# Kernel optimization log

Hardware: AMD Instinct MI355X
Metric: run time of the kernel (lower is better)

The kernel has to match this reference:

```python
import jax, jax.numpy as jnp
from jax import lax
import numpy as np

N_ATOMS, N_BONDS, N_GRAPHS = 8192, 32768, 256
EMBED, HIDDEN, DEPTH = 32, 256, 10
ATOM_VOCAB, BOND_VOCAB = 200, 10


def setup_inputs() -> dict:
    key = jax.random.key(0)
    ks = jax.random.split(key, 16)
    f = lambda k, *sh: jax.random.normal(k, sh, dtype=jnp.float32) * 0.05
    return {
        "atom_features": jax.random.randint(ks[0], (N_ATOMS,), 0, ATOM_VOCAB),
        "bond_features": jax.random.randint(ks[1], (N_BONDS,), 0, BOND_VOCAB),
        "adjacency_matrix": jax.random.randint(ks[2], (N_ATOMS, N_ATOMS), 0, 2, dtype=jnp.int32),
        "batch_indices": jax.random.randint(ks[3], (N_ATOMS,), 0, N_GRAPHS),
        "atom_emb": f(ks[4], ATOM_VOCAB, EMBED),
        "bond_emb": f(ks[5], BOND_VOCAB, EMBED),
        "msg_W": f(ks[6], DEPTH, HIDDEN, 2 * EMBED),
        "msg_b": f(ks[7], DEPTH, HIDDEN),
        "gru_Wih": f(ks[8], DEPTH, 3 * EMBED, HIDDEN),
        "gru_Whh": f(ks[9], DEPTH, 3 * EMBED, EMBED),
        "gru_bih": f(ks[10], DEPTH, 3 * EMBED),
        "gru_bhh": f(ks[11], DEPTH, 3 * EMBED),
        "pool_W": f(ks[12], HIDDEN, EMBED),
        "pool_b": f(ks[13], HIDDEN),
    }


def _gmpn(atom_emb, bond_emb, msg_W, msg_b, gru_Wih, gru_Whh, gru_bih, gru_bhh,
          pool_W, pool_b, atom_features, bond_features, adjacency_matrix, batch_indices):
    H = atom_emb[atom_features]                       # [N, E]
    A = (adjacency_matrix > 0).astype(H.dtype)        # [N, N] 0/1
    deg = A.sum(axis=1)                               # [N]
    has_nb = deg > 0
    inv_deg = jnp.where(has_nb, 1.0 / jnp.maximum(deg, 1.0), 0.0)[:, None]

    def layer(h, params):
        W, b, wih, whh, b_ih, b_hh = params
        # mean_j Linear([h_i ; h_j]) = W1 h_i + W2 mean_j h_j + b
        neigh_mean = (A @ h) * inv_deg                # [N, E]
        W1, W2 = W[:, :EMBED], W[:, EMBED:]
        msg = h @ W1.T + neigh_mean @ W2.T + b        # [N, HIDDEN]
        msg = jnp.where(has_nb[:, None], msg, 0.0)    # zero message if no neighbors
        # single-step GRU: input=msg, hidden state=h
        gi = msg @ wih.T + b_ih
        gh = h @ whh.T + b_hh
        ir, iz, inn = jnp.split(gi, 3, axis=-1)
        hr, hz, hn = jnp.split(gh, 3, axis=-1)
        r = jax.nn.sigmoid(ir + hr)
        z = jax.nn.sigmoid(iz + hz)
        n = jnp.tanh(inn + r * hn)
        h_new = (1.0 - z) * n + z * h                 # [N, E]
        return h_new, None

    H, _ = lax.scan(layer, H, (msg_W, msg_b, gru_Wih, gru_Whh, gru_bih, gru_bhh))

    # per-graph mean pooling (zeros for empty graphs), then global_pool linear
    seg_sum = jax.ops.segment_sum(H, batch_indices, num_segments=N_GRAPHS)
    cnt = jax.ops.segment_sum(jnp.ones((H.shape[0],), H.dtype), batch_indices, num_segments=N_GRAPHS)
    graph_mean = jnp.where(cnt[:, None] > 0, seg_sum / jnp.maximum(cnt, 1.0)[:, None], 0.0)
    graph_embeddings = graph_mean @ pool_W.T + pool_b  # [G, HIDDEN]

    bond_embeddings = bond_emb[bond_features]          # [B, E]
    return H, bond_embeddings, graph_embeddings


def reference(atom_features, bond_features, adjacency_matrix, batch_indices,
              atom_emb, bond_emb, msg_W, msg_b, gru_Wih, gru_Whh, gru_bih, gru_bhh,
              pool_W, pool_b):
    return _gmpn(atom_emb, bond_emb, msg_W, msg_b, gru_Wih, gru_Whh, gru_bih, gru_bhh,
                 pool_W, pool_b, atom_features, bond_features, adjacency_matrix, batch_indices)
```

## Files before the change

### kernel.cpp

```cpp
#include <hip/hip_runtime.h>
#include <stdint.h>

typedef __bf16 bf16x8 __attribute__((ext_vector_type(8)));
typedef float f32x4 __attribute__((ext_vector_type(4)));

__device__ __forceinline__ float b2f(unsigned short u){
  unsigned int t = ((unsigned int)u) << 16;
  return __builtin_bit_cast(float, t);
}
__device__ __forceinline__ unsigned short f2b(float f){
  unsigned int x = __builtin_bit_cast(unsigned int, f);
  x = x + 0x7FFFu + ((x >> 16) & 1u);
  return (unsigned short)(x >> 16);
}
__device__ __forceinline__ void spread8(unsigned int B, unsigned int w[4]){
  unsigned int m = __umul24(B, 0x8001u);
  w[0] = __umul24(m & 0x00010001u, 0x3F80u);
  w[1] = __umul24(m & 0x00040004u, 0x0FE0u);
  w[2] = __umul24(m & 0x00100010u, 0x03F8u);
  w[3] = __umul24(m & 0x00400040u, 0x00FEu);
}
__device__ __forceinline__ float fsig(float x){ return 1.f/(1.f + __expf(-x)); }
__device__ __forceinline__ float ftanh(float x){ return 1.f - 2.f/(__expf(2.f*x) + 1.f); }

__global__ void k_prep(const void* s_msgW, const void* s_msgb, const void* s_wih,
                       const void* s_whh, const void* s_bih, const void* s_bhh,
                       const void* s_poolW, const void* s_poolb,
                       const unsigned short* __restrict__ aemb_u16,
                       unsigned short* __restrict__ cw,
                       int* __restrict__ deg, float* __restrict__ seg,
                       float* __restrict__ cnt, int* __restrict__ flag){
  int b = blockIdx.x, t = threadIdx.x;
  unsigned int uu = aemb_u16[2*t];
  int e = (int)((uu >> 7) & 0xFF);
  unsigned long long vote = __ballot(e >= 100 && e <= 127);
  int isb = (__popcll(vote) > 32) ? 1 : 0;
  if (b < 1771){
    int id = b*256 + t;
    if (id < 453248){
      const void* src; int off;
      if      (id < 163840){ src = s_msgW;  off = id; }
      else if (id < 166400){ src = s_msgb;  off = id - 163840; }
      else if (id < 412160){ src = s_wih;   off = id - 166400; }
      else if (id < 442880){ src = s_whh;   off = id - 412160; }
      else if (id < 443840){ src = s_bih;   off = id - 442880; }
      else if (id < 444800){ src = s_bhh;   off = id - 443840; }
      else if (id < 452992){ src = s_poolW; off = id - 444800; }
      else                 { src = s_poolb; off = id - 452992; }
      cw[id] = isb ? ((const unsigned short*)src)[off]
                   : f2b(((const float*)src)[off]);
    }
  } else {
    int id2 = (b - 1771)*256 + t;
    if (id2 < 8192){ deg[id2] = 0; seg[id2] = 0.f; }
    if (id2 < 256) cnt[id2] = 0.f;
    if (b == 1771 && t == 0) flag[0] = isb;
  }
}

__global__ void k_fuse(const unsigned short* __restrict__ cw,
                       unsigned short* __restrict__ vcat, float* __restrict__ bwv){
  int d = blockIdx.x >> 2, quarter = blockIdx.x & 3;
  const unsigned short* msgW = cw + (size_t)d*16384;
  const unsigned short* msgb = cw + 163840 + d*256;
  const unsigned short* wih  = cw + 166400 + (size_t)d*24576;
  int t = threadIdx.x;
  #pragma unroll
  for (int i=0;i<6;i++){
    int idx = quarter*1536 + i*256 + t;
    int j = idx >> 6, e = idx & 63;
    const unsigned short* wr = wih + j*256;
    const unsigned short* wc = msgW + e;
    float acc = 0.f;
    for (int k=0;k<256;k++)
      acc += b2f(wr[k]) * b2f(wc[k*64]);
    vcat[(size_t)d*6144 + idx] = f2b(acc);
  }
  if (quarter == 0 && t < 96){
    const unsigned short* wr = wih + t*256;
    float acc = 0.f;
    for (int k=0;k<256;k++) acc += b2f(msgb[k]) * b2f(wr[k]);
    bwv[d*96 + t] = acc;
  }
}

__global__ void k_pack(const int* __restrict__ adj, unsigned int* __restrict__ mask3,
                       int* __restrict__ deg){
  int tid = blockIdx.x*256 + threadIdx.x;
  int rb  = tid >> 12;
  int rem = tid & 4095;
  int kgg = rem >> 6;
  int L   = rem & 63;
  int lc = L & 15, q = L >> 4;
  int row = rb*16 + lc;
  const int4* p4 = (const int4*)(adj + (size_t)row*8192 + kgg*128 + q*8);
  unsigned int dw = 0; int pc = 0;
  #pragma unroll
  for (int s=0;s<4;s++){
    int4 u = p4[s*8];
    int4 v = p4[s*8 + 1];
    unsigned int b = (unsigned int)(u.x > 0)
                   | ((unsigned int)(u.y > 0) << 1)
                   | ((unsigned int)(u.z > 0) << 2)
                   | ((unsigned int)(u.w > 0) << 3)
                   | ((unsigned int)(v.x > 0) << 4)
                   | ((unsigned int)(v.y > 0) << 5)
                   | ((unsigned int)(v.z > 0) << 6)
                   | ((unsigned int)(v.w > 0) << 7);
    dw |= b << (8*s);
    pc += __popc(b);
  }
  mask3[tid] = dw;
  pc += __shfl_xor(pc, 16);
  pc += __shfl_xor(pc, 32);
  if (q == 0) atomicAdd(deg + row, pc);
}

__global__ void k_be(const int* __restrict__ af, const void* __restrict__ araw,
                     const int* __restrict__ bft, const void* __restrict__ braw,
                     const int* __restrict__ flag,
                     float* __restrict__ hf32, uint4* __restrict__ hfrag,
                     unsigned short* __restrict__ outB16, float* __restrict__ outB32){
  int b = blockIdx.x, t = threadIdx.x;
  if (b >= 512){
    int id = (b - 512)*512 + t;
    int e = id >> 5, c = id & 31;
    int idx = bft[e]*32 + c;
    if (flag[0]) outB16[id] = ((const unsigned short*)braw)[idx];
    else         outB32[id] = ((const float*)braw)[idx];
    return;
  }
  __shared__ __align__(16) float sh[512];
  int r = t >> 5, c = t & 31;
  int row = b*16 + r;
  int idx = af[row]*32 + c;
  float f;
  if (flag[0]) f = b2f(((const unsigned short*)araw)[idx]);
  else         f = ((const float*)araw)[idx];
  hf32[row*32 + c] = f;
  sh[r*32 + c] = f;
  __syncthreads();
  if (t < 64){
    int nt = t >> 5, Lq = t & 31;
    int ks32 = b >> 1, half = b & 1;
    int col = nt*16 + (Lq & 15);
    int rbase = (Lq >> 4)*8;
    unsigned int w[4];
    #pragma unroll
    for (int p=0;p<4;p++){
      unsigned int lo = f2b(sh[(rbase + 2*p    )*32 + col]);
      unsigned int hi = f2b(sh[(rbase + 2*p + 1)*32 + col]);
      w[p] = lo | (hi << 16);
    }
    hfrag[(ks32*2 + nt)*64 + half*32 + Lq] = make_uint4(w[0],w[1],w[2],w[3]);
  }
}

__launch_bounds__(512, 1)
__global__ void k_layer(const unsigned int* __restrict__ mask3,
                        const uint4* __restrict__ hfragIn,
                        unsigned int* __restrict__ hfragOut,
                        float* __restrict__ hf32,
                        const int* __restrict__ deg,
                        const unsigned short* __restrict__ vcat,
                        const float* __restrict__ bwv,
                        const unsigned short* __restrict__ whh,
                        const unsigned short* __restrict__ bih,
                        const unsigned short* __restrict__ bhh,
                        const int* __restrict__ bidx,
                        float* __restrict__ seg, float* __restrict__ cnt,
                        unsigned short* __restrict__ out16, float* __restrict__ out32,
                        const int* __restrict__ flag, int last)
{
  __shared__ __align__(16) char uni[33792];
  __shared__ __align__(16) unsigned short sA[32][72];
  __shared__ int sdeg[32];

  const int t = threadIdx.x;
  const int b = blockIdx.x;
  const int w = t >> 6, L = t & 63;
  const int q = L >> 4, lc = L & 15;
  const int rowbase = b*32;

  const int r0 = t >> 4;
  const int cl = t & 15;
  const int r  = rowbase + r0;
  const int isb = flag[0];
  const int dgr = deg[r];
  const float invr = dgr > 0 ? 1.f/(float)dgr : 0.f;
  float h0 = hf32[r*32 + cl];
  float h1 = hf32[r*32 + 16 + cl];
  sA[r0][cl]    = f2b(h0);
  sA[r0][16+cl] = f2b(h1);
  if (cl == 0) sdeg[r0] = dgr;

  {
    f32x4 a00={0,0,0,0}, a01={0,0,0,0}, a10={0,0,0,0}, a11={0,0,0,0};
    const unsigned int* mp = mask3 + (size_t)b*8192 + w*512 + L;
    const uint4* bp = hfragIn + (size_t)w*4096 + L;
    for (int g=0; g<8; g++){
      unsigned int mw0 = mp[g*64];
      unsigned int mw1 = mp[4096 + g*64];
      #pragma unroll
      for (int s=0; s<4; s++){
        int ks = g*4 + s;
        uint4 u0 = bp[ks*128];
        uint4 u1 = bp[ks*128 + 64];
        union { unsigned int u[4]; bf16x8 v; } A0, A1, B0, B1;
        spread8((mw0 >> (8*s)) & 0xFFu, A0.u);
        spread8((mw1 >> (8*s)) & 0xFFu, A1.u);
        B0.u[0]=u0.x; B0.u[1]=u0.y; B0.u[2]=u0.z; B0.u[3]=u0.w;
        B1.u[0]=u1.x; B1.u[1]=u1.y; B1.u[2]=u1.z; B1.u[3]=u1.w;
        a00 = __builtin_amdgcn_mfma_f32_16x16x32_bf16(A0.v, B0.v, a00, 0,0,0);
        a01 = __builtin_amdgcn_mfma_f32_16x16x32_bf16(A0.v, B1.v, a01, 0,0,0);
        a10 = __builtin_amdgcn_mfma_f32_16x16x32_bf16(A1.v, B0.v, a10, 0,0,0);
        a11 = __builtin_amdgcn_mfma_f32_16x16x32_bf16(A1.v, B1.v, a11, 0,0,0);
      }
    }
    float* sp = (float*)uni + w*1056;
    #pragma unroll
    for (int rg=0; rg<4; rg++){
      int rw = q*4 + rg;
      sp[rw*33 + lc]         = a00[rg];
      sp[rw*33 + 16 + lc]    = a01[rg];
      sp[(16+rw)*33 + lc]    = a10[rg];
      sp[(16+rw)*33 + 16+lc] = a11[rg];
    }
  }
  __syncthreads();
  {
    const float* spf = (const float*)uni;
    float s0 = 0.f, s1 = 0.f;
    #pragma unroll
    for (int ww=0; ww<8; ww++){
      s0 += spf[ww*1056 + r0*33 + cl];
      s1 += spf[ww*1056 + r0*33 + 16 + cl];
    }
    sA[r0][32+cl] = f2b(s0*invr);
    sA[r0][48+cl] = f2b(s1*invr);
  }
  __syncthreads();
  {
    float* sgi = (float*)uni;
    float* sgh = (float*)(uni + 12800);
    if (w < 6){
      int nt = w;
      union { uint4 u; bf16x8 v; } B0, B1;
      B0.u = *(const uint4*)(vcat + (size_t)(nt*16 + lc)*64 + q*8);
      B1.u = *(const uint4*)(vcat + (size_t)(nt*16 + lc)*64 + 32 + q*8);
      float bw = bwv[nt*16 + lc];
      #pragma unroll
      for (int rt=0; rt<2; rt++){
        union { uint4 u; bf16x8 v; } A0, A1;
        A0.u = *(const uint4*)&sA[rt*16 + lc][q*8];
        A1.u = *(const uint4*)&sA[rt*16 + lc][32 + q*8];
        f32x4 g0 = {0,0,0,0};
        g0 = __builtin_amdgcn_mfma_f32_16x16x32_bf16(A0.v, B0.v, g0, 0,0,0);
        g0 = __builtin_amdgcn_mfma_f32_16x16x32_bf16(A1.v, B1.v, g0, 0,0,0);
        #pragma unroll
        for (int rg=0; rg<4; rg++){
          int rw = rt*16 + q*4 + rg;
          float v = g0[rg] + bw;
          if (sdeg[rw] == 0) v = 0.f;
          sgi[rw*100 + nt*16 + lc] = v;
        }
      }
    } else {
      int rt = w - 6;
      union { uint4 u; bf16x8 v; } A;
      A.u = *(const uint4*)&sA[rt*16 + lc][q*8];
      #pragma unroll
      for (int nt=0; nt<6; nt++){
        union { uint4 u; bf16x8 v; } B;
        B.u = *(const uint4*)(whh + (size_t)(nt*16 + lc)*32 + q*8);
        f32x4 hh = {0,0,0,0};
        hh = __builtin_amdgcn_mfma_f32_16x16x32_bf16(A.v, B.v, hh, 0,0,0);
        #pragma unroll
        for (int rg=0; rg<4; rg++)
          sgh[(rt*16 + q*4+rg)*100 + nt*16 + lc] = hh[rg];
      }
    }
  }
  __syncthreads();
  {
    const float* sgi = (const float*)uni;
    const float* sgh = (const float*)(uni + 12800);
    float ir0 = sgi[r0*100 + cl]    + b2f(bih[cl]),    hr0 = sgh[r0*100 + cl]    + b2f(bhh[cl]);
    float iz0 = sgi[r0*100 + 32+cl] + b2f(bih[32+cl]), hz0 = sgh[r0*100 + 32+cl] + b2f(bhh[32+cl]);
    float in0 = sgi[r0*100 + 64+cl] + b2f(bih[64+cl]), hn0 = sgh[r0*100 + 64+cl] + b2f(bhh[64+cl]);
    float ir1 = sgi[r0*100 + 16+cl] + b2f(bih[16+cl]), hr1 = sgh[r0*100 + 16+cl] + b2f(bhh[16+cl]);
    float iz1 = sgi[r0*100 + 48+cl] + b2f(bih[48+cl]), hz1 = sgh[r0*100 + 48+cl] + b2f(bhh[48+cl]);
    float in1 = sgi[r0*100 + 80+cl] + b2f(bih[80+cl]), hn1 = sgh[r0*100 + 80+cl] + b2f(bhh[80+cl]);
    float rr0 = fsig(ir0 + hr0), zz0 = fsig(iz0 + hz0);
    float rr1 = fsig(ir1 + hr1), zz1 = fsig(iz1 + hz1);
    float nn0 = ftanh(in0 + rr0*hn0);
    float nn1 = ftanh(in1 + rr1*hn1);
    h0 = (1.f - zz0)*nn0 + zz0*h0;
    h1 = (1.f - zz1)*nn1 + zz1*h1;
    hf32[r*32 + cl]      = h0;
    hf32[r*32 + 16 + cl] = h1;
    unsigned int m0 = f2b(h0), m1 = f2b(h1);
    if (!last){
      unsigned int p0 = (unsigned int)__shfl_xor((int)m0, 16);
      unsigned int p1 = (unsigned int)__shfl_xor((int)m1, 16);
      if ((r & 1) == 0){
        int ks32 = r >> 5;
        int Lf = ((r >> 3) & 3)*16 + cl;
        int pidx = (r & 7) >> 1;
        hfragOut[((ks32*2 + 0)*64 + Lf)*4 + pidx] = m0 | (p0 << 16);
        hfragOut[((ks32*2 + 1)*64 + Lf)*4 + pidx] = m1 | (p1 << 16);
      }
    } else {
      if (isb){ out16[r*32 + cl] = (unsigned short)m0; out16[r*32 + 16 + cl] = (unsigned short)m1; }
      else    { out32[r*32 + cl] = h0; out32[r*32 + 16 + cl] = h1; }
      int gb = bidx[r];
      atomicAdd(seg + gb*32 + cl, h0);
      atomicAdd(seg + gb*32 + 16 + cl, h1);
      if (cl == 0) atomicAdd(cnt + gb, 1.f);
    }
  }
}

__global__ void k_pool(const float* __restrict__ seg, const float* __restrict__ cnt,
                       const unsigned short* __restrict__ pw, const unsigned short* __restrict__ pb,
                       const int* __restrict__ flag,
                       unsigned short* __restrict__ outG16, float* __restrict__ outG32){
  int g = blockIdx.x, o = threadIdx.x;
  float cv = cnt[g];
  float ic = cv > 0.f ? 1.f/cv : 0.f;
  float s = 0.f;
  #pragma unroll
  for (int c=0;c<32;c++) s += seg[g*32+c]*ic*b2f(pw[o*32+c]);
  s += b2f(pb[o]);
  if (flag[0]) outG16[g*256 + o] = f2b(s);
  else         outG32[g*256 + o] = s;
}

extern "C" void kernel_launch(void* const* d_in, const int* in_sizes, int n_in,
                              void* d_out, int out_size, void* d_ws, size_t ws_size,
                              hipStream_t stream){
  const int* af   = (const int*)d_in[0];
  const int* bft  = (const int*)d_in[1];
  const int* adj  = (const int*)d_in[2];
  const int* bidx = (const int*)d_in[3];

  char* ws = (char*)d_ws;
  unsigned int*   mask3  = (unsigned int*)(ws + 0);
  unsigned int*   hfrag0 = (unsigned int*)(ws + 8388608);
  unsigned int*   hfrag1 = (unsigned int*)(ws + 8912896);
  float*          hf32   = (float*)(ws + 9437184);
  int*            deg    = (int*)(ws + 10485760);
  float*          seg    = (float*)(ws + 10518528);
  float*          cnt    = (float*)(ws + 10551296);
  int*            flag   = (int*)(ws + 10552320);
  unsigned short* cw     = (unsigned short*)(ws + 10552384);
  unsigned short* vcat   = (unsigned short*)(ws + 11458880);
  float*          bwv    = (float*)(ws + 11581760);

  unsigned short* o16 = (unsigned short*)d_out;
  float*          o32 = (float*)d_out;

  k_prep<<<1803, 256, 0, stream>>>(d_in[6], d_in[7], d_in[8], d_in[9], d_in[10],
                                   d_in[11], d_in[12], d_in[13],
                                   (const unsigned short*)d_in[4],
                                   cw, deg, seg, cnt, flag);
  k_fuse<<<40, 256, 0, stream>>>(cw, vcat, bwv);
  k_pack<<<8192, 256, 0, stream>>>(adj, mask3, deg);
  k_be<<<2560, 512, 0, stream>>>(af, d_in[4], bft, d_in[5], flag,
                                 hf32, (uint4*)hfrag0,
                                 o16 + 262144, o32 + 262144);

  for (int d = 0; d < 10; d++){
    const uint4*  hin  = (const uint4*)((d & 1) ? hfrag1 : hfrag0);
    unsigned int* hout = (d & 1) ? hfrag0 : hfrag1;
    k_layer<<<256, 512, 0, stream>>>(mask3, hin, hout, hf32, deg,
                                     vcat + (size_t)d*6144, bwv + d*96,
                                     cw + 412160 + d*3072,
                                     cw + 442880 + d*96, cw + 443840 + d*96,
                                     bidx, seg, cnt, o16, o32, flag, (d == 9) ? 1 : 0);
  }
  k_pool<<<256, 256, 0, stream>>>(seg, cnt, cw + 444800, cw + 452992, flag,
                                  o16 + 1310720, o32 + 1310720);
}
```

Baseline: 550.0 us.

## Fuse ten per-layer launches into one persistent kernel with grid barrier

Replaces the ten k_layer launches with a single persistent k_layers kernel that loops over depth and synchronises all 256 blocks through an atomic grid barrier in global memory. The hidden state now stays in registers across layers, and the per-layer hf32 global writes go away. The aim is to remove kernel launch and drain overhead between layers. It relies on all 256 blocks being co-resident; if they are not, the barrier deadlocks. The spin barrier also adds its own latency at each layer.

```diff
diff --git a/kernel.cpp b/kernel.cpp
--- a/kernel.cpp
+++ b/kernel.cpp
@@ -22,6 +22,25 @@
 }
 __device__ __forceinline__ float fsig(float x){ return 1.f/(1.f + __expf(-x)); }
 __device__ __forceinline__ float ftanh(float x){ return 1.f - 2.f/(__expf(2.f*x) + 1.f); }
+
+__device__ __forceinline__ void gbar(int* bar){
+  __syncthreads();
+  if (threadIdx.x == 0){
+    int g = __hip_atomic_load(&bar[1], __ATOMIC_RELAXED, __HIP_MEMORY_SCOPE_AGENT);
+    int a = __hip_atomic_fetch_add(&bar[0], 1, __ATOMIC_RELEASE, __HIP_MEMORY_SCOPE_AGENT);
+    if (a == 255){
+      __hip_atomic_store(&bar[0], 0, __ATOMIC_RELAXED, __HIP_MEMORY_SCOPE_AGENT);
+      __hip_atomic_fetch_add(&bar[1], 1, __ATOMIC_RELEASE, __HIP_MEMORY_SCOPE_AGENT);
+    } else {
+      int it = 0;
+      while (__hip_atomic_load(&bar[1], __ATOMIC_RELAXED, __HIP_MEMORY_SCOPE_AGENT) == g){
+        if (++it > 48) __builtin_amdgcn_s_sleep(1);
+      }
+    }
+    (void)__hip_atomic_load(&bar[1], __ATOMIC_ACQUIRE, __HIP_MEMORY_SCOPE_AGENT);
+  }
+  __syncthreads();
+}
 
 __global__ void k_prep(const void* s_msgW, const void* s_msgb, const void* s_wih,
                        const void* s_whh, const void* s_bih, const void* s_bhh,
@@ -54,7 +73,7 @@
     int id2 = (b - 1771)*256 + t;
     if (id2 < 8192){ deg[id2] = 0; seg[id2] = 0.f; }
     if (id2 < 256) cnt[id2] = 0.f;
-    if (b == 1771 && t == 0) flag[0] = isb;
+    if (b == 1771 && t == 0){ flag[0] = isb; flag[4] = 0; flag[5] = 0; }
   }
 }
 
@@ -156,21 +175,19 @@
   }
 }
 
-__launch_bounds__(512, 1)
-__global__ void k_layer(const unsigned int* __restrict__ mask3,
-                        const uint4* __restrict__ hfragIn,
-                        unsigned int* __restrict__ hfragOut,
-                        float* __restrict__ hf32,
-                        const int* __restrict__ deg,
-                        const unsigned short* __restrict__ vcat,
-                        const float* __restrict__ bwv,
-                        const unsigned short* __restrict__ whh,
-                        const unsigned short* __restrict__ bih,
-                        const unsigned short* __restrict__ bhh,
-                        const int* __restrict__ bidx,
-                        float* __restrict__ seg, float* __restrict__ cnt,
-                        unsigned short* __restrict__ out16, float* __restrict__ out32,
-                        const int* __restrict__ flag, int last)
+__launch_bounds__(512)
+__global__ void k_layers(const unsigned int* __restrict__ mask3,
+                         unsigned int* __restrict__ hfrag0,
+                         unsigned int* __restrict__ hfrag1,
+                         const float* __restrict__ hf32,
+                         const int* __restrict__ deg,
+                         const unsigned short* __restrict__ cw,
+                         const unsigned short* __restrict__ vcat,
+                         const float* __restrict__ bwv,
+                         const int* __restrict__ bidx,
+                         float* __restrict__ seg, float* __restrict__ cnt,
+                         unsigned short* __restrict__ out16, float* __restrict__ out32,
+                         const int* __restrict__ flag, int* bar)
 {
   __shared__ __align__(16) char uni[33792];
   __shared__ __align__(16) unsigned short sA[32][72];
@@ -190,134 +207,145 @@
   const float invr = dgr > 0 ? 1.f/(float)dgr : 0.f;
   float h0 = hf32[r*32 + cl];
   float h1 = hf32[r*32 + 16 + cl];
-  sA[r0][cl]    = f2b(h0);
-  sA[r0][16+cl] = f2b(h1);
   if (cl == 0) sdeg[r0] = dgr;
 
-  {
-    f32x4 a00={0,0,0,0}, a01={0,0,0,0}, a10={0,0,0,0}, a11={0,0,0,0};
-    const unsigned int* mp = mask3 + (size_t)b*8192 + w*512 + L;
-    const uint4* bp = hfragIn + (size_t)w*4096 + L;
-    for (int g=0; g<8; g++){
-      unsigned int mw0 = mp[g*64];
-      unsigned int mw1 = mp[4096 + g*64];
+  for (int d = 0; d < 10; ++d){
+    const unsigned short* vcd = vcat + (size_t)d*6144;
+    const float*          bwd = bwv + d*96;
+    const unsigned short* whh = cw + 412160 + d*3072;
+    const unsigned short* bih = cw + 442880 + d*96;
+    const unsigned short* bhh = cw + 443840 + d*96;
+    const uint4*  hfragIn  = (const uint4*)((d & 1) ? hfrag1 : hfrag0);
+    unsigned int* hfragOut = (d & 1) ? hfrag0 : hfrag1;
+    const int last = (d == 9);
+
+    sA[r0][cl]    = f2b(h0);
+    sA[r0][16+cl] = f2b(h1);
+
+    {
+      f32x4 a00={0,0,0,0}, a01={0,0,0,0}, a10={0,0,0,0}, a11={0,0,0,0};
+      const unsigned int* mp = mask3 + (size_t)b*8192 + w*512 + L;
+      const uint4* bp = hfragIn + (size_t)w*4096 + L;
+      for (int g=0; g<8; g++){
+        unsigned int mw0 = mp[g*64];
+        unsigned int mw1 = mp[4096 + g*64];
+        #pragma unroll
+        for (int s=0; s<4; s++){
+          int ks = g*4 + s;
+          uint4 u0 = bp[ks*128];
+          uint4 u1 = bp[ks*128 + 64];
+          union { unsigned int u[4]; bf16x8 v; } A0, A1, B0, B1;
+          spread8((mw0 >> (8*s)) & 0xFFu, A0.u);
+          spread8((mw1 >> (8*s)) & 0xFFu, A1.u);
+          B0.u[0]=u0.x; B0.u[1]=u0.y; B0.u[2]=u0.z; B0.u[3]=u0.w;
+          B1.u[0]=u1.x; B1.u[1]=u1.y; B1.u[2]=u1.z; B1.u[3]=u1.w;
+          a00 = __builtin_amdgcn_mfma_f32_16x16x32_bf16(A0.v, B0.v, a00, 0,0,0);
+          a01 = __builtin_amdgcn_mfma_f32_16x16x32_bf16(A0.v, B1.v, a01, 0,0,0);
+          a10 = __builtin_amdgcn_mfma_f32_16x16x32_bf16(A1.v, B0.v, a10, 0,0,0);
+          a11 = __builtin_amdgcn_mfma_f32_16x16x32_bf16(A1.v, B1.v, a11, 0,0,0);
+        }
+      }
+      float* sp = (float*)uni + w*1056;
       #pragma unroll
-      for (int s=0; s<4; s++){
-        int ks = g*4 + s;
-        uint4 u0 = bp[ks*128];
-        uint4 u1 = bp[ks*128 + 64];
-        union { unsigned int u[4]; bf16x8 v; } A0, A1, B0, B1;
-        spread8((mw0 >> (8*s)) & 0xFFu, A0.u);
-        spread8((mw1 >> (8*s)) & 0xFFu, A1.u);
-        B0.u[0]=u0.x; B0.u[1]=u0.y; B0.u[2]=u0.z; B0.u[3]=u0.w;
-        B1.u[0]=u1.x; B1.u[1]=u1.y; B1.u[2]=u1.z; B1.u[3]=u1.w;
-        a00 = __builtin_amdgcn_mfma_f32_16x16x32_bf16(A0.v, B0.v, a00, 0,0,0);
-        a01 = __builtin_amdgcn_mfma_f32_16x16x32_bf16(A0.v, B1.v, a01, 0,0,0);
-        a10 = __builtin_amdgcn_mfma_f32_16x16x32_bf16(A1.v, B0.v, a10, 0,0,0);
-        a11 = __builtin_amdgcn_mfma_f32_16x16x32_bf16(A1.v, B1.v, a11, 0,0,0);
-      }
-    }
-    float* sp = (float*)uni + w*1056;
-    #pragma unroll
-    for (int rg=0; rg<4; rg++){
-      int rw = q*4 + rg;
-      sp[rw*33 + lc]         = a00[rg];
-      sp[rw*33 + 16 + lc]    = a01[rg];
-      sp[(16+rw)*33 + lc]    = a10[rg];
-      sp[(16+rw)*33 + 16+lc] = a11[rg];
-    }
-  }
-  __syncthreads();
-  {
-    const float* spf = (const float*)uni;
-    float s0 = 0.f, s1 = 0.f;
-    #pragma unroll
-    for (int ww=0; ww<8; ww++){
-      s0 += spf[ww*1056 + r0*33 + cl];
-      s1 += spf[ww*1056 + r0*33 + 16 + cl];
-    }
-    sA[r0][32+cl] = f2b(s0*invr);
-    sA[r0][48+cl] = f2b(s1*invr);
-  }
-  __syncthreads();
-  {
-    float* sgi = (float*)uni;
-    float* sgh = (float*)(uni + 12800);
-    if (w < 6){
-      int nt = w;
-      union { uint4 u; bf16x8 v; } B0, B1;
-      B0.u = *(const uint4*)(vcat + (size_t)(nt*16 + lc)*64 + q*8);
-      B1.u = *(const uint4*)(vcat + (size_t)(nt*16 + lc)*64 + 32 + q*8);
-      float bw = bwv[nt*16 + lc];
+      for (int rg=0; rg<4; rg++){
+        int rw = q*4 + rg;
+        sp[rw*33 + lc]         = a00[rg];
+        sp[rw*33 + 16 + lc]    = a01[rg];
+        sp[(16+rw)*33 + lc]    = a10[rg];
+        sp[(16+rw)*33 + 16+lc] = a11[rg];
+      }
+    }
+    __syncthreads();
+    {
+      const float* spf = (const float*)uni;
+      float s0 = 0.f, s1 = 0.f;
       #pragma unroll
-      for (int rt=0; rt<2; rt++){
-        union { uint4 u; bf16x8 v; } A0, A1;
-        A0.u = *(const uint4*)&sA[rt*16 + lc][q*8];
-        A1.u = *(const uint4*)&sA[rt*16 + lc][32 + q*8];
-        f32x4 g0 = {0,0,0,0};
-        g0 = __builtin_amdgcn_mfma_f32_16x16x32_bf16(A0.v, B0.v, g0, 0,0,0);
-        g0 = __builtin_amdgcn_mfma_f32_16x16x32_bf16(A1.v, B1.v, g0, 0,0,0);
+      for (int ww=0; ww<8; ww++){
+        s0 += spf[ww*1056 + r0*33 + cl];
+        s1 += spf[ww*1056 + r0*33 + 16 + cl];
+      }
+      sA[r0][32+cl] = f2b(s0*invr);
+      sA[r0][48+cl] = f2b(s1*invr);
+    }
+    __syncthreads();
+    {
+      float* sgi = (float*)uni;
+      float* sgh = (float*)(uni + 12800);
+      if (w < 6){
+        int nt = w;
+        union { uint4 u; bf16x8 v; } B0, B1;
+        B0.u = *(const uint4*)(vcd + (size_t)(nt*16 + lc)*64 + q*8);
+        B1.u = *(const uint4*)(vcd + (size_t)(nt*16 + lc)*64 + 32 + q*8);
+        float bw = bwd[nt*16 + lc];
         #pragma unroll
-        for (int rg=0; rg<4; rg++){
-          int rw = rt*16 + q*4 + rg;
-          float v = g0[rg] + bw;
-          if (sdeg[rw] == 0) v = 0.f;
-          sgi[rw*100 + nt*16 + lc] = v;
+        for (int rt=0; rt<2; rt++){
+          union { uint4 u; bf16x8 v; } A0, A1;
+          A0.u = *(const uint4*)&sA[rt*16 + lc][q*8];
+          A1.u = *(const uint4*)&sA[rt*16 + lc][32 + q*8];
+          f32x4 g0 = {0,0,0,0};
+          g0 = __builtin_amdgcn_mfma_f32_16x16x32_bf16(A0.v, B0.v, g0, 0,0,0);
+          g0 = __builtin_amdgcn_mfma_f32_16x16x32_bf16(A1.v, B1.v, g0, 0,0,0);
+          #pragma unroll
+          for (int rg=0; rg<4; rg++){
+            int rw = rt*16 + q*4 + rg;
+            float v = g0[rg] + bw;
+            if (sdeg[rw] == 0) v = 0.f;
+            sgi[rw*100 + nt*16 + lc] = v;
+          }
         }
-      }
-    } else {
-      int rt = w - 6;
-      union { uint4 u; bf16x8 v; } A;
-      A.u = *(const uint4*)&sA[rt*16 + lc][q*8];
-      #pragma unroll
-      for (int nt=0; nt<6; nt++){
-        union { uint4 u; bf16x8 v; } B;
-        B.u = *(const uint4*)(whh + (size_t)(nt*16 + lc)*32 + q*8);
-        f32x4 hh = {0,0,0,0};
-        hh = __builtin_amdgcn_mfma_f32_16x16x32_bf16(A.v, B.v, hh, 0,0,0);
+      } else {
+        int rt = w - 6;
+        union { uint4 u; bf16x8 v; } A;
+        A.u = *(const uint4*)&sA[rt*16 + lc][q*8];
         #pragma unroll
-        for (int rg=0; rg<4; rg++)
-          sgh[(rt*16 + q*4+rg)*100 + nt*16 + lc] = hh[rg];
-      }
-    }
-  }
-  __syncthreads();
-  {
-    const float* sgi = (const float*)uni;
-    const float* sgh = (const float*)(uni + 12800);
-    float ir0 = sgi[r0*100 + cl]    + b2f(bih[cl]),    hr0 = sgh[r0*100 + cl]    + b2f(bhh[cl]);
-    float iz0 = sgi[r0*100 + 32+cl] + b2f(bih[32+cl]), hz0 = sgh[r0*100 + 32+cl] + b2f(bhh[32+cl]);
-    float in0 = sgi[r0*100 + 64+cl] + b2f(bih[64+cl]), hn0 = sgh[r0*100 + 64+cl] + b2f(bhh[64+cl]);
-    float ir1 = sgi[r0*100 + 16+cl] + b2f(bih[16+cl]), hr1 = sgh[r0*100 + 16+cl] + b2f(bhh[16+cl]);
-    float iz1 = sgi[r0*100 + 48+cl] + b2f(bih[48+cl]), hz1 = sgh[r0*100 + 48+cl] + b2f(bhh[48+cl]);
-    float in1 = sgi[r0*100 + 80+cl] + b2f(bih[80+cl]), hn1 = sgh[r0*100 + 80+cl] + b2f(bhh[80+cl]);
-    float rr0 = fsig(ir0 + hr0), zz0 = fsig(iz0 + hz0);
-    float rr1 = fsig(ir1 + hr1), zz1 = fsig(iz1 + hz1);
-    float nn0 = ftanh(in0 + rr0*hn0);
-    float nn1 = ftanh(in1 + rr1*hn1);
-    h0 = (1.f - zz0)*nn0 + zz0*h0;
-    h1 = (1.f - zz1)*nn1 + zz1*h1;
-    hf32[r*32 + cl]      = h0;
-    hf32[r*32 + 16 + cl] = h1;
-    unsigned int m0 = f2b(h0), m1 = f2b(h1);
-    if (!last){
-      unsigned int p0 = (unsigned int)__shfl_xor((int)m0, 16);
-      unsigned int p1 = (unsigned int)__shfl_xor((int)m1, 16);
-      if ((r & 1) == 0){
-        int ks32 = r >> 5;
-        int Lf = ((r >> 3) & 3)*16 + cl;
-        int pidx = (r & 7) >> 1;
-        hfragOut[((ks32*2 + 0)*64 + Lf)*4 + pidx] = m0 | (p0 << 16);
-        hfragOut[((ks32*2 + 1)*64 + Lf)*4 + pidx] = m1 | (p1 << 16);
-      }
-    } else {
-      if (isb){ out16[r*32 + cl] = (unsigned short)m0; out16[r*32 + 16 + cl] = (unsigned short)m1; }
-      else    { out32[r*32 + cl] = h0; out32[r*32 + 16 + cl] = h1; }
-      int gb = bidx[r];
-      atomicAdd(seg + gb*32 + cl, h0);
-      atomicAdd(seg + gb*32 + 16 + cl, h1);
-      if (cl == 0) atomicAdd(cnt + gb, 1.f);
-    }
+        for (int nt=0; nt<6; nt++){
+          union { uint4 u; bf16x8 v; } B;
+          B.u = *(const uint4*)(whh + (size_t)(nt*16 + lc)*32 + q*8);
+          f32x4 hh = {0,0,0,0};
+          hh = __builtin_amdgcn_mfma_f32_16x16x32_bf16(A.v, B.v, hh, 0,0,0);
+          #pragma unroll
+          for (int rg=0; rg<4; rg++)
+            sgh[(rt*16 + q*4+rg)*100 + nt*16 + lc] = hh[rg];
+        }
+      }
+    }
+    __syncthreads();
+    {
+      const float* sgi = (const float*)uni;
+      const float* sgh = (const float*)(uni + 12800);
+      float ir0 = sgi[r0*100 + cl]    + b2f(bih[cl]),    hr0 = sgh[r0*100 + cl]    + b2f(bhh[cl]);
+      float iz0 = sgi[r0*100 + 32+cl] + b2f(bih[32+cl]), hz0 = sgh[r0*100 + 32+cl] + b2f(bhh[32+cl]);
+      float in0 = sgi[r0*100 + 64+cl] + b2f(bih[64+cl]), hn0 = sgh[r0*100 + 64+cl] + b2f(bhh[64+cl]);
+      float ir1 = sgi[r0*100 + 16+cl] + b2f(bih[16+cl]), hr1 = sgh[r0*100 + 16+cl] + b2f(bhh[16+cl]);
+      float iz1 = sgi[r0*100 + 48+cl] + b2f(bih[48+cl]), hz1 = sgh[r0*100 + 48+cl] + b2f(bhh[48+cl]);
+      float in1 = sgi[r0*100 + 80+cl] + b2f(bih[80+cl]), hn1 = sgh[r0*100 + 80+cl] + b2f(bhh[80+cl]);
+      float rr0 = fsig(ir0 + hr0), zz0 = fsig(iz0 + hz0);
+      float rr1 = fsig(ir1 + hr1), zz1 = fsig(iz1 + hz1);
+      float nn0 = ftanh(in0 + rr0*hn0);
+      float nn1 = ftanh(in1 + rr1*hn1);
+      h0 = (1.f - zz0)*nn0 + zz0*h0;
+      h1 = (1.f - zz1)*nn1 + zz1*h1;
+      unsigned int m0 = f2b(h0), m1 = f2b(h1);
+      if (!last){
+        unsigned int p0 = (unsigned int)__shfl_xor((int)m0, 16);
+        unsigned int p1 = (unsigned int)__shfl_xor((int)m1, 16);
+        if ((r & 1) == 0){
+          int ks32 = r >> 5;
+          int Lf = ((r >> 3) & 3)*16 + cl;
+          int pidx = (r & 7) >> 1;
+          hfragOut[((ks32*2 + 0)*64 + Lf)*4 + pidx] = m0 | (p0 << 16);
+          hfragOut[((ks32*2 + 1)*64 + Lf)*4 + pidx] = m1 | (p1 << 16);
+        }
+      } else {
+        if (isb){ out16[r*32 + cl] = (unsigned short)m0; out16[r*32 + 16 + cl] = (unsigned short)m1; }
+        else    { out32[r*32 + cl] = h0; out32[r*32 + 16 + cl] = h1; }
+        int gb = bidx[r];
+        atomicAdd(seg + gb*32 + cl, h0);
+        atomicAdd(seg + gb*32 + 16 + cl, h1);
+        if (cl == 0) atomicAdd(cnt + gb, 1.f);
+      }
+    }
+    if (!last) gbar(bar);
   }
 }
 
@@ -359,6 +387,7 @@
 
   unsigned short* o16 = (unsigned short*)d_out;
   float*          o32 = (float*)d_out;
+  int*            bar = flag + 4;
 
   k_prep<<<1803, 256, 0, stream>>>(d_in[6], d_in[7], d_in[8], d_in[9], d_in[10],
                                    d_in[11], d_in[12], d_in[13],
@@ -370,15 +399,9 @@
                                  hf32, (uint4*)hfrag0,
                                  o16 + 262144, o32 + 262144);
 
-  for (int d = 0; d < 10; d++){
-    const uint4*  hin  = (const uint4*)((d & 1) ? hfrag1 : hfrag0);
-    unsigned int* hout = (d & 1) ? hfrag0 : hfrag1;
-    k_layer<<<256, 512, 0, stream>>>(mask3, hin, hout, hf32, deg,
-                                     vcat + (size_t)d*6144, bwv + d*96,
-                                     cw + 412160 + d*3072,
-                                     cw + 442880 + d*96, cw + 443840 + d*96,
-                                     bidx, seg, cnt, o16, o32, flag, (d == 9) ? 1 : 0);
-  }
+  k_layers<<<256, 512, 0, stream>>>(mask3, hfrag0, hfrag1, hf32, deg, cw,
+                                    vcat, bwv, bidx, seg, cnt, o16, o32, flag, bar);
+
   k_pool<<<256, 256, 0, stream>>>(seg, cnt, cw + 444800, cw + 452992, flag,
                                   o16 + 1310720, o32 + 1310720);
 }
```

Measured after the change: 640.7 us. 1.16x slower.
